# Performance work log

Hardware: AMD Instinct MI355X
Metric: run time of the kernel (lower is better)

Reference implementation:

```python
import jax, jax.numpy as jnp
import numpy as np

B, T = 32, 128
D, H, HD = 512, 8, 64
FF, E, N = 2048, 8, 3
NF = 16            # Fourier features
VOCAB, FEAT = 119, 200
SCALE = 10.0
EPS = 1e-5


def layernorm(x, g, b):
    m = jnp.mean(x, axis=-1, keepdims=True)
    v = jnp.mean((x - m) ** 2, axis=-1, keepdims=True)
    return (x - m) * jax.lax.rsqrt(v + EPS) * g + b


def setup_inputs() -> dict:
    key = jax.random.key(0)
    ks = jax.random.split(key, 32)
    f32 = jnp.float32
    inp = {
        "src": jax.random.randint(ks[0], (B, T), 0, VOCAB),
        "frac": jax.random.uniform(ks[1], (B, T), dtype=f32),
        "embed_table": jax.random.normal(ks[2], (VOCAB, FEAT), f32),
        "W_m2v": jax.random.normal(ks[3], (FEAT, D), f32) * 0.05,
        "b_m2v": jnp.zeros((D,), f32),
        "pb_W": jax.random.normal(ks[4], (1, NF), f32) * 0.1,
        "pb_b": jax.random.uniform(ks[5], (NF,), f32) * 2 * np.pi,
        "pb_a": jax.random.normal(ks[6], (NF,), f32),
        "Wk": jax.random.normal(ks[7], (N, D, D), f32) * 0.03,
        "bk": jnp.zeros((N, D), f32),
        "Wv": jax.random.normal(ks[8], (N, D, D), f32) * 0.03,
        "bv": jnp.zeros((N, D), f32),
        "Wo": jax.random.normal(ks[9], (N, D, D), f32) * 0.03,
        "bo": jnp.zeros((N, D), f32),
        "ln1_g": jnp.ones((N, D), f32),
        "ln1_b": jnp.zeros((N, D), f32),
        "ln2_g": jnp.ones((N, D), f32),
        "ln2_b": jnp.zeros((N, D), f32),
        "gate_W": jax.random.normal(ks[10], (N, D, E), f32) * 0.05,
        "gate_b": jnp.zeros((N, E), f32),
        "eW1": jax.random.normal(ks[11], (N, E, D, FF), f32) * 0.03,
        "eb1": jnp.zeros((N, E, FF), f32),
        "eW2": jax.random.normal(ks[12], (N, E, FF, D), f32) * 0.02,
        "eb2": jnp.zeros((N, E, D), f32),
    }
    return inp


def reference(src, frac, embed_table, W_m2v, b_m2v, pb_W, pb_b, pb_a,
              Wk, bk, Wv, bv, Wo, bo, ln1_g, ln1_b, ln2_g, ln2_b,
              gate_W, gate_b, eW1, eb1, eW2, eb2):
    # Embedder: mat2vec lookup + linear projection
    x = embed_table[src] @ W_m2v + b_m2v                      # [B,T,D]

    # Fourier positional bias: pb[b,i,j] = cos((frac_j - frac_i)*scale * W + b) @ a
    diffs = (frac[:, None, :] - frac[:, :, None]) * SCALE     # [B,T,T]
    rff = jnp.cos(diffs[..., None] * pb_W[0] + pb_b)          # [B,T,T,NF]
    pb = rff @ pb_a                                           # [B,T,T]

    for i in range(N):
        # --- Fourier-bias attention ---
        K = (x @ Wk[i] + bk[i]).reshape(B, T, H, HD).transpose(0, 2, 1, 3)  # [B,H,T,HD]
        V = (x @ Wv[i] + bv[i]).reshape(B, T, H, HD).transpose(0, 2, 1, 3)
        # scores[b,h,i,j,d] = K[b,h,j,d] + pb[b,i,j]; weighted = sum_j scores*V
        # factor: sum_j K*V (indep of i) + sum_j pb[b,i,j]*V[b,h,j,d]
        kv = jnp.sum(K * V, axis=2)                           # [B,H,HD]
        pbv = jnp.einsum('bij,bhjd->bhid', pb, V)             # [B,H,T,HD]
        wv = (pbv + kv[:, :, None, :]).transpose(0, 2, 1, 3).reshape(B, T, D)
        x = layernorm(x + wv @ Wo[i] + bo[i], ln1_g[i], ln1_b[i])

        # --- MoE FFN, top-2 gating (eval mode: no dropout/noise) ---
        probs = jax.nn.softmax(x @ gate_W[i] + gate_b[i], axis=-1)   # [B,T,E]
        top2_s, top2_e = jax.lax.top_k(probs, 2)                     # [B,T,2]
        w = jnp.sum(jax.nn.one_hot(top2_e, E, dtype=x.dtype) * top2_s[..., None], axis=2)  # [B,T,E]
        h = jax.nn.relu(jnp.einsum('btd,edf->btef', x, eW1[i]) + eb1[i])  # [B,T,E,FF]
        eo = jnp.einsum('btef,efd->bted', h, eW2[i]) + eb2[i]             # [B,T,E,D]
        ff = jnp.einsum('bte,bted->btd', w, eo)
        x = layernorm(x + ff, ln2_g[i], ln2_b[i])
    return x
```

## Files before the change

### kernel.cpp

```cpp
#include <hip/hip_runtime.h>
#include <math.h>

#define B_    32
#define T_    128
#define D_    512
#define FF_   2048
#define E_    8
#define NL_   3
#define NF_   16
#define FEAT_ 200
#define BT_   4096

#define GB_   64
#define TPB_  (BT_ / GB_)

typedef short bf16x8 __attribute__((ext_vector_type(8)));
typedef float f32x4  __attribute__((ext_vector_type(4)));

__device__ inline unsigned short f2bf(float f) {
    unsigned u = __float_as_uint(f);
    unsigned r = (u + 0x7fffu + ((u >> 16) & 1u)) >> 16;
    return (unsigned short)r;
}
__device__ inline void split_bf(float f, unsigned short& h, unsigned short& l) {
    h = f2bf(f);
    float fh = __uint_as_float(((unsigned)h) << 16);
    l = f2bf(f - fh);
}

__device__ __forceinline__ void ld_g2l(const unsigned short* g, unsigned short* l)
{
    __builtin_amdgcn_global_load_lds(
        (const __attribute__((address_space(1))) unsigned int*)(uintptr_t)g,
        (__attribute__((address_space(3))) unsigned int*)(uintptr_t)l,
        16, 0, 0);
}

template <int MODE, bool SPLITOUT, bool RELU>
__global__ __launch_bounds__(256)
void mgemm_k(const unsigned short* __restrict__ Ah, const unsigned short* __restrict__ Al,
             const unsigned short* __restrict__ Bh, const unsigned short* __restrict__ Bl,
             const float* __restrict__ bias,
             float* __restrict__ Cf, unsigned short* __restrict__ Ch,
             unsigned short* __restrict__ Cl,
             int M, int K, int N, long strB, int strBias,
             const int* __restrict__ counts, const int* __restrict__ offsets,
             const int* __restrict__ tok_list)
{
    const int z  = blockIdx.z;
    const int m0 = blockIdx.y * 128, n0 = blockIdx.x * 128;
    int rows, rowoff = 0;
    if constexpr (MODE != 0) {
        rows = counts[z];
        if (m0 >= rows) return;
        rowoff = offsets[z];
    } else {
        rows = M;
    }
    const unsigned short* Bhb = Bh + (long)z * strB;
    const unsigned short* Blb = Bl + (long)z * strB;
    const float* biasb = bias + (long)z * strBias;

    __shared__ unsigned short S[2][4 * 4096];

    const int tid  = threadIdx.x;
    const int w    = tid >> 6, lane = tid & 63;
    const int wm = w & 1, wn = w >> 1;
    const int l15 = lane & 15, quad = lane >> 4;

    const int lrow0 = w * 32 + (lane >> 2);
    const int lrow1 = lrow0 + 16;
    const int sseg  = (lane & 3) ^ ((lane >> 3) & 3);
    const int lb0   = (w * 2 + 0) * 512;
    const int lb1   = (w * 2 + 1) * 512;

    long ga0, ga1;
    if constexpr (MODE == 1) {
        int m_a = m0 + lrow0; if (m_a >= rows) m_a = rows - 1;
        int m_b = m0 + lrow1; if (m_b >= rows) m_b = rows - 1;
        ga0 = tok_list[z * BT_ + m_a];
        ga1 = tok_list[z * BT_ + m_b];
    } else if constexpr (MODE == 2) {
        int m_a = m0 + lrow0; if (m_a >= rows) m_a = rows - 1;
        int m_b = m0 + lrow1; if (m_b >= rows) m_b = rows - 1;
        ga0 = (long)rowoff + m_a;
        ga1 = (long)rowoff + m_b;
    } else {
        ga0 = m0 + lrow0;
        ga1 = m0 + lrow1;
    }
    const long aoff0 = ga0 * (long)K + sseg * 8;
    const long aoff1 = ga1 * (long)K + sseg * 8;
    const long boff0 = (long)(n0 + lrow0) * K + sseg * 8;
    const long boff1 = (long)(n0 + lrow1) * K + sseg * 8;

    f32x4 acc[4][4];
#pragma unroll
    for (int i = 0; i < 4; ++i)
#pragma unroll
        for (int j = 0; j < 4; ++j) acc[i][j] = (f32x4)0.f;

    const int xq = quad ^ ((l15 >> 1) & 3);

    {
        unsigned short* Sb = S[0];
        ld_g2l(Ah  + aoff0, Sb + 0 * 4096 + lb0);
        ld_g2l(Ah  + aoff1, Sb + 0 * 4096 + lb1);
        ld_g2l(Al  + aoff0, Sb + 1 * 4096 + lb0);
        ld_g2l(Al  + aoff1, Sb + 1 * 4096 + lb1);
        ld_g2l(Bhb + boff0, Sb + 2 * 4096 + lb0);
        ld_g2l(Bhb + boff1, Sb + 2 * 4096 + lb1);
        ld_g2l(Blb + boff0, Sb + 3 * 4096 + lb0);
        ld_g2l(Blb + boff1, Sb + 3 * 4096 + lb1);
    }

    unsigned short* Scur = S[0];
    unsigned short* Snxt = S[1];

    for (int k0 = 0; k0 < K; k0 += 32) {
        __syncthreads();

        if (k0 + 32 < K) {
            int kn = k0 + 32;
            ld_g2l(Ah  + aoff0 + kn, Snxt + 0 * 4096 + lb0);
            ld_g2l(Ah  + aoff1 + kn, Snxt + 0 * 4096 + lb1);
            ld_g2l(Al  + aoff0 + kn, Snxt + 1 * 4096 + lb0);
            ld_g2l(Al  + aoff1 + kn, Snxt + 1 * 4096 + lb1);
            ld_g2l(Bhb + boff0 + kn, Snxt + 2 * 4096 + lb0);
            ld_g2l(Bhb + boff1 + kn, Snxt + 2 * 4096 + lb1);
            ld_g2l(Blb + boff0 + kn, Snxt + 3 * 4096 + lb0);
            ld_g2l(Blb + boff1 + kn, Snxt + 3 * 4096 + lb1);
        }

        bf16x8 ah4[4], al4[4], bh4[4], bl4[4];
#pragma unroll
        for (int i = 0; i < 4; ++i) {
            int ro = (wm * 64 + i * 16 + l15) * 32 + xq * 8;
            ah4[i] = *(const bf16x8*)&Scur[0 * 4096 + ro];
            al4[i] = *(const bf16x8*)&Scur[1 * 4096 + ro];
        }
#pragma unroll
        for (int j = 0; j < 4; ++j) {
            int ro = (wn * 64 + j * 16 + l15) * 32 + xq * 8;
            bh4[j] = *(const bf16x8*)&Scur[2 * 4096 + ro];
            bl4[j] = *(const bf16x8*)&Scur[3 * 4096 + ro];
        }
#pragma unroll
        for (int i = 0; i < 4; ++i)
#pragma unroll
            for (int j = 0; j < 4; ++j) {
                acc[i][j] = __builtin_amdgcn_mfma_f32_16x16x32_bf16(al4[i], bh4[j], acc[i][j], 0, 0, 0);
                acc[i][j] = __builtin_amdgcn_mfma_f32_16x16x32_bf16(ah4[i], bl4[j], acc[i][j], 0, 0, 0);
                acc[i][j] = __builtin_amdgcn_mfma_f32_16x16x32_bf16(ah4[i], bh4[j], acc[i][j], 0, 0, 0);
            }

        unsigned short* t = Scur; Scur = Snxt; Snxt = t;
    }

#pragma unroll
    for (int i = 0; i < 4; ++i) {
#pragma unroll
        for (int r = 0; r < 4; ++r) {
            int gm = m0 + wm * 64 + i * 16 + quad * 4 + r;
            if (MODE != 0 && gm >= rows) continue;
            long crow = (MODE != 0) ? ((long)rowoff + gm) : (long)gm;
#pragma unroll
            for (int j = 0; j < 4; ++j) {
                int col = n0 + wn * 64 + j * 16 + l15;
                float v = acc[i][j][r] + biasb[col];
                if constexpr (RELU) v = fmaxf(v, 0.f);
                if constexpr (SPLITOUT) {
                    unsigned short h, l;
                    split_bf(v, h, l);
                    Ch[crow * (long)N + col] = h;
                    Cl[crow * (long)N + col] = l;
                } else {
                    Cf[crow * (long)N + col] = v;
                }
            }
        }
    }
}

template <bool WF32, bool SPLIT>
__global__ __launch_bounds__(256)
void gemm_k(const float* __restrict__ A, const float* __restrict__ Bm,
            const float* __restrict__ bias, float* __restrict__ C,
            unsigned short* __restrict__ Oh, unsigned short* __restrict__ Ol,
            int K, int lda, int ldb, int ldc,
            long strA, long strB, long strC, int strBias)
{
    const int z  = blockIdx.z;
    const int m0 = blockIdx.y * 64, n0 = blockIdx.x * 64;
    const float* Ab    = A    + (long)z * strA;
    const float* Bb    = Bm   + (long)z * strB;
    const float* biasb = bias + (long)z * strBias;

    __shared__ float As[16][68];
    __shared__ float Bs[16][64];

    const int tid = threadIdx.x;
    const int tx  = tid & 15, ty = tid >> 4;
    const int ar  = tid >> 2;
    const int akc = (tid & 3) * 4;
    const float* Arow = Ab + (long)(m0 + ar) * lda;
    const int bkr = tid >> 4;
    const int bnc = (tid & 15) * 4;

    float acc[4][4];
#pragma unroll
    for (int i = 0; i < 4; ++i)
#pragma unroll
        for (int j = 0; j < 4; ++j) acc[i][j] = 0.f;

    for (int k0 = 0; k0 < K; k0 += 16) {
        if (k0 + 16 <= K) {
            float4 a = *(const float4*)(Arow + k0 + akc);
            As[akc + 0][ar] = a.x; As[akc + 1][ar] = a.y;
            As[akc + 2][ar] = a.z; As[akc + 3][ar] = a.w;
        } else {
#pragma unroll
            for (int j = 0; j < 4; ++j) {
                int kk = k0 + akc + j;
                As[akc + j][ar] = (kk < K) ? Arow[kk] : 0.f;
            }
        }
        {
            int kk = k0 + bkr;
            float4 b;
            if (kk < K) b = *(const float4*)(Bb + (long)kk * ldb + n0 + bnc);
            else        b = make_float4(0.f, 0.f, 0.f, 0.f);
            *(float4*)&Bs[bkr][bnc] = b;
        }
        __syncthreads();
#pragma unroll
        for (int k = 0; k < 16; ++k) {
            float4 av = *(const float4*)&As[k][ty * 4];
            float4 bv = *(const float4*)&Bs[k][tx * 4];
            float am[4] = {av.x, av.y, av.z, av.w};
            float bn[4] = {bv.x, bv.y, bv.z, bv.w};
#pragma unroll
            for (int i = 0; i < 4; ++i)
#pragma unroll
                for (int j = 0; j < 4; ++j)
                    acc[i][j] = fmaf(am[i], bn[j], acc[i][j]);
        }
        __syncthreads();
    }
#pragma unroll
    for (int i = 0; i < 4; ++i) {
        long base = ((long)z * strC) + (long)(m0 + ty * 4 + i) * ldc + n0 + tx * 4;
        const float* bp = biasb + n0 + tx * 4;
#pragma unroll
        for (int j = 0; j < 4; ++j) {
            float v = acc[i][j] + bp[j];
            if constexpr (WF32) C[base + j] = v;
            if constexpr (SPLIT) {
                unsigned short h, l;
                split_bf(v, h, l);
                Oh[base + j] = h;
                Ol[base + j] = l;
            }
        }
    }
}

__global__ __launch_bounds__(256)
void transpose_split_k(const float* __restrict__ in,
                       unsigned short* __restrict__ oh, unsigned short* __restrict__ ol,
                       int R, int C, long strIn, long strOut)
{
    __shared__ float tile[32][33];
    const float* I = in + (long)blockIdx.z * strIn;
    unsigned short* OH = oh + (long)blockIdx.z * strOut;
    unsigned short* OL = ol + (long)blockIdx.z * strOut;
    int c0 = blockIdx.x * 32, r0 = blockIdx.y * 32;
    int tx = threadIdx.x & 31, ty = threadIdx.x >> 5;
#pragma unroll
    for (int i = 0; i < 4; ++i)
        tile[ty + i * 8][tx] = I[(long)(r0 + ty + i * 8) * C + c0 + tx];
    __syncthreads();
#pragma unroll
    for (int i = 0; i < 4; ++i) {
        unsigned short h, l;
        split_bf(tile[tx][ty + i * 8], h, l);
        long o = (long)(c0 + ty + i * 8) * R + r0 + tx;
        OH[o] = h; OL[o] = l;
    }
}

__global__ void bias_cat_k(const float* __restrict__ a, const float* __restrict__ b,
                           float* __restrict__ o)
{
    int i = blockIdx.x * 256 + threadIdx.x;
    o[i] = (i < D_) ? a[i] : b[i - D_];
}

__global__ void embed_gather_k(const int* __restrict__ src,
                               const float* __restrict__ table,
                               float* __restrict__ emb)
{
    int t = blockIdx.x;
    int v = src[t];
    for (int k = threadIdx.x; k < FEAT_; k += 256)
        emb[t * FEAT_ + k] = table[v * FEAT_ + k];
}

__global__ __launch_bounds__(256)
void pb_k(const float* __restrict__ frac, const float* __restrict__ pbW,
          const float* __restrict__ pbb, const float* __restrict__ pba,
          float* __restrict__ pb)
{
    int idx = blockIdx.x * 256 + threadIdx.x;
    int b = idx >> 14;
    int i = (idx >> 7) & 127;
    int j = idx & 127;
    float diff = (frac[b * T_ + j] - frac[b * T_ + i]) * 10.0f;
    float s = 0.f;
#pragma unroll
    for (int f = 0; f < NF_; ++f)
        s = fmaf(cosf(fmaf(diff, pbW[f], pbb[f])), pba[f], s);
    pb[idx] = s;
}

__global__ __launch_bounds__(256)
void kv_k(const float* __restrict__ KV, float* __restrict__ kv)
{
    int idx = blockIdx.x * 256 + threadIdx.x;
    int b = idx >> 9, c = idx & 511;
    const float* Kp = KV + (long)b * T_ * 1024 + c;
    float s = 0.f;
    for (int t = 0; t < T_; ++t) {
        const float* p = Kp + t * 1024;
        s = fmaf(p[0], p[D_], s);
    }
    kv[idx] = s;
}

__global__ __launch_bounds__(256)
void ln_res_k(const float* __restrict__ x, const float* __restrict__ add,
              const float* __restrict__ g, const float* __restrict__ b,
              float* __restrict__ out, unsigned short* __restrict__ oh,
              unsigned short* __restrict__ ol)
{
    int wave = threadIdx.x >> 6, lane = threadIdx.x & 63;
    int row = blockIdx.x * 4 + wave;
    const float* xr = x   + (long)row * D_ + lane * 8;
    const float* ar = add + (long)row * D_ + lane * 8;
    float v[8]; float s = 0.f;
#pragma unroll
    for (int j = 0; j < 8; ++j) { v[j] = xr[j] + ar[j]; s += v[j]; }
#pragma unroll
    for (int off = 32; off > 0; off >>= 1) s += __shfl_xor(s, off, 64);
    float mean = s * (1.f / D_);
    float q = 0.f;
#pragma unroll
    for (int j = 0; j < 8; ++j) { float d = v[j] - mean; q += d * d; }
#pragma unroll
    for (int off = 32; off > 0; off >>= 1) q += __shfl_xor(q, off, 64);
    float inv = rsqrtf(q * (1.f / D_) + 1e-5f);
    float* orow = out + (long)row * D_ + lane * 8;
    unsigned short* hrow = oh + (long)row * D_ + lane * 8;
    unsigned short* lrow = ol + (long)row * D_ + lane * 8;
#pragma unroll
    for (int j = 0; j < 8; ++j) {
        int c = lane * 8 + j;
        float o = (v[j] - mean) * inv * g[c] + b[c];
        orow[j] = o;
        unsigned short hh, ll;
        split_bf(o, hh, ll);
        hrow[j] = hh; lrow[j] = ll;
    }
}

__global__ __launch_bounds__(256)
void ln_moe_k(const float* __restrict__ x, const float* __restrict__ eo,
              const int* __restrict__ tok_slot, const float* __restrict__ tok_w,
              const int* __restrict__ offsets,
              const float* __restrict__ g, const float* __restrict__ b,
              float* __restrict__ out, unsigned short* __restrict__ oh,
              unsigned short* __restrict__ ol)
{
    int wave = threadIdx.x >> 6, lane = threadIdx.x & 63;
    int row = blockIdx.x * 4 + wave;
    int  c0 = tok_slot[row * 2], c1 = tok_slot[row * 2 + 1];
    float w0 = tok_w[row * 2],  w1 = tok_w[row * 2 + 1];
    long r0 = offsets[c0 >> 12] + (c0 & 4095);
    long r1 = offsets[c1 >> 12] + (c1 & 4095);
    const float* xr = x  + (long)row * D_ + lane * 8;
    const float* e0 = eo + r0 * D_ + lane * 8;
    const float* e1 = eo + r1 * D_ + lane * 8;
    float v[8]; float s = 0.f;
#pragma unroll
    for (int j = 0; j < 8; ++j) {
        v[j] = xr[j] + w0 * e0[j] + w1 * e1[j];
        s += v[j];
    }
#pragma unroll
    for (int off = 32; off > 0; off >>= 1) s += __shfl_xor(s, off, 64);
    float mean = s * (1.f / D_);
    float q = 0.f;
#pragma unroll
    for (int j = 0; j < 8; ++j) { float d = v[j] - mean; q += d * d; }
#pragma unroll
    for (int off = 32; off > 0; off >>= 1) q += __shfl_xor(q, off, 64);
    float inv = rsqrtf(q * (1.f / D_) + 1e-5f);
    float* orow = out + (long)row * D_ + lane * 8;
    unsigned short* hrow = oh + (long)row * D_ + lane * 8;
    unsigned short* lrow = ol + (long)row * D_ + lane * 8;
#pragma unroll
    for (int j = 0; j < 8; ++j) {
        int c = lane * 8 + j;
        float o = (v[j] - mean) * inv * g[c] + b[c];
        orow[j] = o;
        unsigned short hh, ll;
        split_bf(o, hh, ll);
        hrow[j] = hh; lrow[j] = ll;
    }
}

__global__ __launch_bounds__(256)
void gate_k(const float* __restrict__ x, const float* __restrict__ gW,
            const float* __restrict__ gb, int* __restrict__ counts,
            int* __restrict__ tok_list, int* __restrict__ tok_slot,
            float* __restrict__ tok_w)
{
    __shared__ int scnt[E_];
    __shared__ int sbase[E_];
    __shared__ int sent[TPB_][2];

    const int wave = threadIdx.x >> 6, lane = threadIdx.x & 63;
    const int e  = lane & 7;
    const int ch = lane >> 3;
    const int t0 = blockIdx.x * TPB_;

    if (threadIdx.x < E_) scnt[threadIdx.x] = 0;
    __syncthreads();

    for (int it = 0; it < TPB_ / 4; ++it) {
        const int tl = it * 4 + wave;
        const int t  = t0 + tl;

        const float4* x4 = (const float4*)(x + (long)t * D_ + ch * 64);
        const float*  wr = gW + (long)ch * 64 * E_ + e;
        float acc = 0.f;
#pragma unroll
        for (int d4 = 0; d4 < 16; ++d4) {
            float4 xv = x4[d4];
            acc = fmaf(xv.x, wr[(d4 * 4 + 0) * 8], acc);
            acc = fmaf(xv.y, wr[(d4 * 4 + 1) * 8], acc);
            acc = fmaf(xv.z, wr[(d4 * 4 + 2) * 8], acc);
            acc = fmaf(xv.w, wr[(d4 * 4 + 3) * 8], acc);
        }
        acc += __shfl_xor(acc, 8, 64);
        acc += __shfl_xor(acc, 16, 64);
        acc += __shfl_xor(acc, 32, 64);
        acc += gb[e];

        float lg[8];
#pragma unroll
        for (int ee = 0; ee < 8; ++ee)
            lg[ee] = __shfl(acc, (lane & 56) | ee, 64);

        float m = lg[0];
#pragma unroll
        for (int ee = 1; ee < 8; ++ee) m = fmaxf(m, lg[ee]);
        float p[8]; float s = 0.f;
#pragma unroll
        for (int ee = 0; ee < 8; ++ee) { p[ee] = expf(lg[ee] - m); s += p[ee]; }
        float inv = 1.f / s;
        int e1 = 0;
#pragma unroll
        for (int ee = 1; ee < 8; ++ee) if (p[ee] > p[e1]) e1 = ee;
        int e2 = (e1 == 0) ? 1 : 0;
#pragma unroll
        for (int ee = 0; ee < 8; ++ee) {
            if (ee == e1) continue;
            if (p[ee] > p[e2]) e2 = ee;
        }

        if (lane == 0) {
            int ls1 = atomicAdd(&scnt[e1], 1);
            int ls2 = atomicAdd(&scnt[e2], 1);
            sent[tl][0] = (e1 << 12) | ls1;
            sent[tl][1] = (e2 << 12) | ls2;
            tok_w[t * 2]     = p[e1] * inv;
            tok_w[t * 2 + 1] = p[e2] * inv;
        }
    }
    __syncthreads();

    if (threadIdx.x < E_)
        sbase[threadIdx.x] = atomicAdd(&counts[threadIdx.x], scnt[threadIdx.x]);
    __syncthreads();

    for (int tl = threadIdx.x; tl < TPB_; tl += 256) {
        const int t = t0 + tl;
#pragma unroll
        for (int kk = 0; kk < 2; ++kk) {
            int v    = sent[tl][kk];
            int ee   = v >> 12;
            int slot = sbase[ee] + (v & 4095);
            tok_list[ee * BT_ + slot] = t;
            tok_slot[t * 2 + kk] = (ee << 12) | slot;
        }
    }
}

__global__ void zero_counts_k(int* __restrict__ counts)
{
    if (threadIdx.x < E_) counts[threadIdx.x] = 0;
}

__global__ void scan_k(const int* __restrict__ counts, int* __restrict__ offsets)
{
    if (threadIdx.x == 0) {
        int s = 0;
        for (int e = 0; e < E_; ++e) { offsets[e] = s; s += counts[e]; }
    }
}

extern "C" void kernel_launch(void* const* d_in, const int* in_sizes, int n_in,
                              void* d_out, int out_size, void* d_ws, size_t ws_size,
                              hipStream_t stream)
{
    const int*   src   = (const int*)  d_in[0];
    const float* frac  = (const float*)d_in[1];
    const float* table = (const float*)d_in[2];
    const float* W_m2v = (const float*)d_in[3];
    const float* b_m2v = (const float*)d_in[4];
    const float* pbW   = (const float*)d_in[5];
    const float* pbb   = (const float*)d_in[6];
    const float* pba   = (const float*)d_in[7];
    const float* Wk    = (const float*)d_in[8];
    const float* bk    = (const float*)d_in[9];
    const float* Wv    = (const float*)d_in[10];
    const float* bv    = (const float*)d_in[11];
    const float* Wo    = (const float*)d_in[12];
    const float* bo    = (const float*)d_in[13];
    const float* ln1g  = (const float*)d_in[14];
    const float* ln1b  = (const float*)d_in[15];
    const float* ln2g  = (const float*)d_in[16];
    const float* ln2b  = (const float*)d_in[17];
    const float* gW    = (const float*)d_in[18];
    const float* gb    = (const float*)d_in[19];
    const float* eW1   = (const float*)d_in[20];
    const float* eb1   = (const float*)d_in[21];
    const float* eW2   = (const float*)d_in[22];
    const float* eb2   = (const float*)d_in[23];

    float* ws   = (float*)d_ws;
    float* x    = ws;  ws += (long)BT_ * D_;
    float* pb   = ws;  ws += (long)B_ * T_ * T_;
    float* eo   = ws;  ws += (long)2 * BT_ * D_;
    float* kv   = ws;  ws += B_ * D_;
    float* tokw = ws;  ws += 2 * BT_;
    float* kvbias = ws; ws += 2 * D_;
    unsigned short* us = (unsigned short*)ws;
    unsigned short* x_h   = us;  us += (long)BT_ * D_;
    unsigned short* x_l   = us;  us += (long)BT_ * D_;
    unsigned short* Wkv_h = us;  us += (long)2 * D_ * D_;
    unsigned short* Wkv_l = us;  us += (long)2 * D_ * D_;
    unsigned short* Wo_h  = us;  us += (long)D_ * D_;
    unsigned short* Wo_l  = us;  us += (long)D_ * D_;
    unsigned short* e1_h  = us;  us += (long)E_ * FF_ * D_;
    unsigned short* e1_l  = us;  us += (long)E_ * FF_ * D_;
    unsigned short* e2_h  = us;  us += (long)E_ * D_ * FF_;
    unsigned short* e2_l  = us;  us += (long)E_ * D_ * FF_;
    int* counts  = (int*)us;
    int* offsets = counts + 8;
    int* toklist = offsets + 8;
    int* tokslot = toklist + E_ * BT_;
    char* ar = (char*)(tokslot + 2 * BT_);
    ar = (char*)(((size_t)ar + 255) & ~(size_t)255);
    unsigned short* h_h = (unsigned short*)ar;
    unsigned short* h_l = h_h + (long)2 * BT_ * FF_;
    float* emb  = (float*)ar;
    float* KVb  = emb + (long)BT_ * FEAT_;
    float* tmp  = KVb + (long)BT_ * 2 * D_;
    unsigned short* wv_h = (unsigned short*)(tmp + (long)BT_ * D_);
    unsigned short* wv_l = wv_h + (long)BT_ * D_;

    embed_gather_k<<<BT_, 256, 0, stream>>>(src, table, emb);
    gemm_k<true, true><<<dim3(8, 64, 1), 256, 0, stream>>>(
        emb, W_m2v, b_m2v, x, x_h, x_l, FEAT_, FEAT_, D_, D_, 0, 0, 0, 0);

    pb_k<<<(B_ * T_ * T_) / 256, 256, 0, stream>>>(frac, pbW, pbb, pba, pb);

    for (int i = 0; i < NL_; ++i) {
        transpose_split_k<<<dim3(16, 16, 1), 256, 0, stream>>>(
            Wk + (long)i * D_ * D_, Wkv_h, Wkv_l, D_, D_, 0, 0);
        transpose_split_k<<<dim3(16, 16, 1), 256, 0, stream>>>(
            Wv + (long)i * D_ * D_, Wkv_h + (long)D_ * D_, Wkv_l + (long)D_ * D_,
            D_, D_, 0, 0);
        transpose_split_k<<<dim3(16, 16, 1), 256, 0, stream>>>(
            Wo + (long)i * D_ * D_, Wo_h, Wo_l, D_, D_, 0, 0);
        transpose_split_k<<<dim3(64, 16, E_), 256, 0, stream>>>(
            eW1 + (long)i * E_ * D_ * FF_, e1_h, e1_l, D_, FF_,
            (long)D_ * FF_, (long)FF_ * D_);
        transpose_split_k<<<dim3(16, 64, E_), 256, 0, stream>>>(
            eW2 + (long)i * E_ * FF_ * D_, e2_h, e2_l, FF_, D_,
            (long)FF_ * D_, (long)D_ * FF_);
        bias_cat_k<<<4, 256, 0, stream>>>(bk + i * D_, bv + i * D_, kvbias);

        mgemm_k<0, false, false><<<dim3(8, 32, 1), 256, 0, stream>>>(
            x_h, x_l, Wkv_h, Wkv_l, kvbias,
            KVb, nullptr, nullptr, BT_, D_, 2 * D_, 0, 0,
            nullptr, nullptr, nullptr);

        kv_k<<<(B_ * D_) / 256, 256, 0, stream>>>(KVb, kv);

        gemm_k<false, true><<<dim3(8, 2, B_), 256, 0, stream>>>(
            pb, KVb + D_, kv, nullptr, wv_h, wv_l, T_, T_, 2 * D_, D_,
            (long)T_ * T_, (long)T_ * 2 * D_, (long)T_ * D_, D_);

        mgemm_k<0, false, false><<<dim3(4, 32, 1), 256, 0, stream>>>(
            wv_h, wv_l, Wo_h, Wo_l, bo + i * D_,
            tmp, nullptr, nullptr, BT_, D_, D_, 0, 0, nullptr, nullptr, nullptr);

        ln_res_k<<<BT_ / 4, 256, 0, stream>>>(x, tmp, ln1g + i * D_, ln1b + i * D_,
                                              x, x_h, x_l);

        zero_counts_k<<<1, 64, 0, stream>>>(counts);
        gate_k<<<GB_, 256, 0, stream>>>(x, gW + (long)i * D_ * E_, gb + i * E_,
                                        counts, toklist, tokslot, tokw);
        scan_k<<<1, 1, 0, stream>>>(counts, offsets);

        mgemm_k<1, true, true><<<dim3(16, 32, E_), 256, 0, stream>>>(
            x_h, x_l, e1_h, e1_l, eb1 + (long)i * E_ * FF_,
            nullptr, h_h, h_l, 0, D_, FF_,
            (long)FF_ * D_, FF_, counts, offsets, toklist);
        mgemm_k<2, false, false><<<dim3(4, 32, E_), 256, 0, stream>>>(
            h_h, h_l, e2_h, e2_l, eb2 + (long)i * E_ * D_,
            eo, nullptr, nullptr, 0, FF_, D_,
            (long)D_ * FF_, D_, counts, offsets, toklist);

        float* dst = (i == NL_ - 1) ? (float*)d_out : x;
        ln_moe_k<<<BT_ / 4, 256, 0, stream>>>(x, eo, tokslot, tokw, offsets,
                                              ln2g + i * D_, ln2b + i * D_,
                                              dst, x_h, x_l);
    }
}
```

Before: 1.216 ms.

## Pre-gather routed tokens into contiguous buffers and remap GEMM blocks across XCDs

Adds a gather kernel that copies each routed token's split-bf16 activations into a contiguous per-expert buffer. The first expert GEMM can then read A rows directly (mode 2) instead of indirecting through the token list. It also remaps block indices in the GEMM so that consecutive blocks on the same XCD share nearby M/expert tiles, aiming to improve L2 reuse. The cost is an extra gather kernel and a reuse of the eo buffer as scratch for the gathered activations.

```diff
diff --git a/kernel.cpp b/kernel.cpp
--- a/kernel.cpp
+++ b/kernel.cpp
@@ -47,8 +47,20 @@
              const int* __restrict__ counts, const int* __restrict__ offsets,
              const int* __restrict__ tok_list)
 {
-    const int z  = blockIdx.z;
-    const int m0 = blockIdx.y * 128, n0 = blockIdx.x * 128;
+    int bn = blockIdx.x, bm = blockIdx.y, bz = blockIdx.z;
+    {
+        const int gx = gridDim.x, gy = gridDim.y, gz = gridDim.z;
+        if (((gy * gz) & 7) == 0) {
+            int lin = bn + gx * (bm + gy * bz);
+            int xcd = lin & 7, r = lin >> 3;
+            bn = r % gx;
+            int g = xcd + 8 * (r / gx);
+            bm = g % gy;
+            bz = g / gy;
+        }
+    }
+    const int z  = bz;
+    const int m0 = bm * 128, n0 = bn * 128;
     int rows, rowoff = 0;
     if constexpr (MODE != 0) {
         rows = counts[z];
@@ -505,6 +517,23 @@
             tok_slot[t * 2 + kk] = (ee << 12) | slot;
         }
     }
+}
+
+__global__ __launch_bounds__(256)
+void gather_tok_k(const unsigned short* __restrict__ xh,
+                  const unsigned short* __restrict__ xl,
+                  const int* __restrict__ tok_slot, const int* __restrict__ offsets,
+                  unsigned short* __restrict__ xgh, unsigned short* __restrict__ xgl)
+{
+    int wid  = blockIdx.x * 4 + (threadIdx.x >> 6);
+    int lane = threadIdx.x & 63;
+    int t = wid >> 1, k = wid & 1;
+    int c = tok_slot[t * 2 + k];
+    long r = offsets[c >> 12] + (c & 4095);
+    const bf16x8* sh = (const bf16x8*)(xh + (long)t * D_);
+    const bf16x8* sl = (const bf16x8*)(xl + (long)t * D_);
+    ((bf16x8*)(xgh + r * D_))[lane] = sh[lane];
+    ((bf16x8*)(xgl + r * D_))[lane] = sl[lane];
 }
 
 __global__ void zero_counts_k(int* __restrict__ counts)
@@ -571,6 +600,8 @@
     int* offsets = counts + 8;
     int* toklist = offsets + 8;
     int* tokslot = toklist + E_ * BT_;
+    unsigned short* xg_h = (unsigned short*)eo;
+    unsigned short* xg_l = xg_h + (long)2 * BT_ * D_;
     char* ar = (char*)(tokslot + 2 * BT_);
     ar = (char*)(((size_t)ar + 255) & ~(size_t)255);
     unsigned short* h_h = (unsigned short*)ar;
@@ -626,8 +657,11 @@
                                         counts, toklist, tokslot, tokw);
         scan_k<<<1, 1, 0, stream>>>(counts, offsets);
 
-        mgemm_k<1, true, true><<<dim3(16, 32, E_), 256, 0, stream>>>(
-            x_h, x_l, e1_h, e1_l, eb1 + (long)i * E_ * FF_,
+        gather_tok_k<<<(2 * BT_) / 4, 256, 0, stream>>>(
+            x_h, x_l, tokslot, offsets, xg_h, xg_l);
+
+        mgemm_k<2, true, true><<<dim3(16, 32, E_), 256, 0, stream>>>(
+            xg_h, xg_l, e1_h, e1_l, eb1 + (long)i * E_ * FF_,
             nullptr, h_h, h_l, 0, D_, FF_,
             (long)FF_ * D_, FF_, counts, offsets, toklist);
         mgemm_k<2, false, false><<<dim3(4, 32, E_), 256, 0, stream>>>(
```

Result: slower. 1.290 ms (+6.1%).
